# Optimization experiments

Measured on AMD Instinct MI355X. Metric: run time of the kernel, lower is better.

## Reference

```python
import jax, jax.numpy as jnp
import numpy as np

B, N, DEG, E, Hd, IT = 512, 81, 20, 16, 96, 4


def sudoku_neighbors():
    # 20 constraint neighbors (row/col/box, excluding self) per cell of a 9x9 grid
    n = 9
    nbrs = []
    for r in range(n):
        for c in range(n):
            s = set()
            for k in range(n):
                s.add(r * n + k)
                s.add(k * n + c)
            br, bc = (r // 3) * 3, (c // 3) * 3
            for dr in range(3):
                for dc in range(3):
                    s.add((br + dr) * n + (bc + dc))
            s.discard(r * n + c)
            nbrs.append(sorted(s))
    return np.asarray(nbrs, dtype=np.int32)  # [81, 20]


def mlp3(x, w1, b1, w2, b2, w3, b3):
    # MLP([in, h, h, out]): ReLU between layers, linear output
    x = jax.nn.relu(x @ w1 + b1)
    x = jax.nn.relu(x @ w2 + b2)
    return x @ w3 + b3


def setup_inputs() -> dict:
    key = jax.random.key(0)
    ks = iter(jax.random.split(key, 64))
    W = lambda shape, s=0.05: jax.random.normal(next(ks), shape, jnp.float32) * s
    inp = {
        'grids': jax.random.randint(next(ks), (B, N), 0, 10),
        'nbr': jnp.asarray(sudoku_neighbors()),
        'iters': IT,
        'c0': jax.random.normal(next(ks), (B * N, Hd), jnp.float32),
        'embed_w': W((10, E), 1.0),
        'in_w1': W((E, Hd)), 'in_b1': jnp.zeros((Hd,)),
        'in_w2': W((Hd, Hd)), 'in_b2': jnp.zeros((Hd,)),
        'in_w3': W((Hd, Hd)), 'in_b3': jnp.zeros((Hd,)),
        'f_w1': W((2 * Hd, Hd)), 'f_b1': jnp.zeros((Hd,)),
        'f_w2': W((Hd, Hd)), 'f_b2': jnp.zeros((Hd,)),
        'f_w3': W((Hd, Hd)), 'f_b3': jnp.zeros((Hd,)),
        'g_w1': W((2 * Hd, Hd)), 'g_b1': jnp.zeros((Hd,)),
        'g_w2': W((Hd, Hd)), 'g_b2': jnp.zeros((Hd,)),
        'g_w3': W((Hd, Hd)), 'g_b3': jnp.zeros((Hd,)),
        'lstm_wih': W((Hd, 4 * Hd)), 'lstm_whh': W((Hd, 4 * Hd)),
        'lstm_bih': jnp.zeros((4 * Hd,)), 'lstm_bhh': jnp.zeros((4 * Hd,)),
        'r_w1': W((Hd, Hd)), 'r_b1': jnp.zeros((Hd,)),
        'r_w2': W((Hd, Hd)), 'r_b2': jnp.zeros((Hd,)),
        'r_w3': W((Hd, E)), 'r_b3': jnp.zeros((E,)),
    }
    return inp


def reference(grids, nbr, iters, c0, embed_w,
              in_w1, in_b1, in_w2, in_b2, in_w3, in_b3,
              f_w1, f_b1, f_w2, f_b2, f_w3, f_b3,
              g_w1, g_b1, g_w2, g_b2, g_w3, g_b3,
              lstm_wih, lstm_whh, lstm_bih, lstm_bhh,
              r_w1, r_b1, r_w2, r_b2, r_w3, r_b3):
    X = mlp3(embed_w[grids], in_w1, in_b1, in_w2, in_b2, in_w3, in_b3)  # [B,N,Hd]
    h0 = jax.lax.stop_gradient(X).reshape(B * N, Hd)  # H = X.clone().detach()
    c = c0  # [B*N, Hd]

    def step(carry, _):
        h, c = carry
        H = h.reshape(B, N, Hd)
        Hn = H[:, nbr]  # gather neighbor states [B,N,DEG,Hd]
        pair = jnp.concatenate(
            [jnp.broadcast_to(H[:, :, None, :], Hn.shape), Hn], axis=-1)  # [B,N,DEG,2Hd]
        M = mlp3(pair, f_w1, f_b1, f_w2, f_b2, f_w3, f_b3).sum(axis=2)  # [B,N,Hd]
        x_in = mlp3(jnp.concatenate([X, M], axis=-1),
                    g_w1, g_b1, g_w2, g_b2, g_w3, g_b3).reshape(B * N, Hd)
        gates = x_in @ lstm_wih + lstm_bih + h @ lstm_whh + lstm_bhh
        i, f, g, o = jnp.split(gates, 4, axis=-1)  # torch gate order i,f,g,o
        c2 = jax.nn.sigmoid(f) * c + jax.nn.sigmoid(i) * jnp.tanh(g)
        h2 = jax.nn.sigmoid(o) * jnp.tanh(c2)
        out = mlp3(h2.reshape(B, N, Hd), r_w1, r_b1, r_w2, r_b2, r_w3, r_b3)
        return (h2, c2), out

    _, outs = jax.lax.scan(step, (h0, c), None, length=iters)
    return outs  # [iters, B, N, E]
```

## Files before the change

### kernel.cpp

```cpp
#include <hip/hip_runtime.h>
#include <math.h>

#define Bsz 512
#define Nc  81
#define Rtot (Bsz*Nc)
#define DEG 20
#define Edim 16
#define HD  96
#define NITER 4

typedef __attribute__((ext_vector_type(8))) __bf16 bf16x8;
typedef __attribute__((ext_vector_type(4))) float f32x4;

__device__ __forceinline__ float sigf(float x){ return 1.0f/(1.0f+__expf(-x)); }
__device__ __forceinline__ float tanh_fast(float x){ return 2.0f/(1.0f+__expf(-2.0f*x)) - 1.0f; }

__device__ __forceinline__ unsigned short f2bf(float f){
    union{float f; unsigned u;} v; v.f=f;
    unsigned r = v.u + 0x7fff + ((v.u>>16)&1);
    return (unsigned short)(r>>16);
}
__device__ __forceinline__ float bf2f(unsigned short s){
    union{unsigned u; float f;} v; v.u=((unsigned)s)<<16; return v.f;
}
__device__ __forceinline__ bf16x8 pack8f(const float* x){
    bf16x8 r;
    #pragma unroll
    for (int j=0;j<8;j++) r[j]=(__bf16)x[j];
    return r;
}
__device__ __forceinline__ bf16x8 ldw(const __bf16* p){ return *(const bf16x8*)p; }

__device__ __forceinline__ int swz(int row, int col){
    return row*96 + ((((col>>2) ^ (row&7))<<2) | (col&3));
}
__device__ __forceinline__ void ldtr8(const float* tp, int row, int c, float* o){
    const int r96 = row*96, rho = row&7;
    const float4 a = *(const float4*)(tp + r96 + ((((c>>2)  ) ^ rho)<<2));
    const float4 b = *(const float4*)(tp + r96 + ((((c>>2)+1) ^ rho)<<2));
    o[0]=a.x;o[1]=a.y;o[2]=a.z;o[3]=a.w;o[4]=b.x;o[5]=b.y;o[6]=b.z;o[7]=b.w;
}
__device__ __forceinline__ bf16x8 packtr8(const float* tp, int row, int c){
    float t[8]; ldtr8(tp,row,c,t); return pack8f(t);
}

#define OFF_FW1T 0
#define OFF_FW2T 18432
#define OFF_FW3T 27648
#define OFF_GW1T 36864
#define OFF_GW2T 55296
#define OFF_GW3T 64512
#define OFF_WIHT 73728
#define OFF_WHHT 110592
#define OFF_RW1T 147456
#define OFF_RW2T 156672
#define OFF_RW3T 165888
#define OFF_IW1T 167424
#define OFF_IW2T 170496
#define OFF_IW3T 179712
#define WT_TOTAL 188928

__global__ __launch_bounds__(256) void k_prep(
    const float* __restrict__ fw1, const float* __restrict__ fw2, const float* __restrict__ fw3,
    const float* __restrict__ gw1, const float* __restrict__ gw2, const float* __restrict__ gw3,
    const float* __restrict__ wih, const float* __restrict__ whh,
    const float* __restrict__ rw1, const float* __restrict__ rw2, const float* __restrict__ rw3,
    const float* __restrict__ iw1, const float* __restrict__ iw2, const float* __restrict__ iw3,
    __bf16* __restrict__ wt)
{
    int i = blockIdx.x*256 + threadIdx.x;
    if (i >= WT_TOTAL) return;
    int j = i;
    if (j < 18432){ int n=j/96, k=j-n*96;
        wt[OFF_FW1T+j] = (__bf16)(n<96 ? fw1[k*96+n] : fw1[(96+k)*96+(n-96)]); return; }
    j -= 18432;
    if (j < 9216){ int n=j/96, k=j-n*96; wt[OFF_FW2T+j]=(__bf16)fw2[k*96+n]; return; }
    j -= 9216;
    if (j < 9216){ int n=j/96, k=j-n*96; wt[OFF_FW3T+j]=(__bf16)fw3[k*96+n]; return; }
    j -= 9216;
    if (j < 18432){ int n=j/192, k=j-n*192; wt[OFF_GW1T+j]=(__bf16)gw1[k*96+n]; return; }
    j -= 18432;
    if (j < 9216){ int n=j/96, k=j-n*96; wt[OFF_GW2T+j]=(__bf16)gw2[k*96+n]; return; }
    j -= 9216;
    if (j < 9216){ int n=j/96, k=j-n*96; wt[OFF_GW3T+j]=(__bf16)gw3[k*96+n]; return; }
    j -= 9216;
    if (j < 36864){ int n=j/96, k=j-n*96; wt[OFF_WIHT+j]=(__bf16)wih[k*384+n]; return; }
    j -= 36864;
    if (j < 36864){ int n=j/96, k=j-n*96; wt[OFF_WHHT+j]=(__bf16)whh[k*384+n]; return; }
    j -= 36864;
    if (j < 9216){ int n=j/96, k=j-n*96; wt[OFF_RW1T+j]=(__bf16)rw1[k*96+n]; return; }
    j -= 9216;
    if (j < 9216){ int n=j/96, k=j-n*96; wt[OFF_RW2T+j]=(__bf16)rw2[k*96+n]; return; }
    j -= 9216;
    if (j < 1536){ int n=j/96, k=j-n*96; wt[OFF_RW3T+j]=(__bf16)rw3[k*16+n]; return; }
    j -= 1536;
    if (j < 3072){ int n=j>>5, k=j&31; wt[OFF_IW1T+j]=(__bf16)iw1[(k&15)*96+n]; return; }
    j -= 3072;
    if (j < 9216){ int n=j/96, k=j-n*96; wt[OFF_IW2T+j]=(__bf16)iw2[k*96+n]; return; }
    j -= 9216;
    { int n=j/96, k=j-n*96; wt[OFF_IW3T+j]=(__bf16)iw3[k*96+n]; }
}

__global__ __launch_bounds__(64) void k_embed2(
    const int* __restrict__ grids, const float* __restrict__ embw,
    const __bf16* __restrict__ wt,
    const float* __restrict__ ib1, const float* __restrict__ ib2, const float* __restrict__ ib3,
    __bf16* __restrict__ X, __bf16* __restrict__ Ag, __bf16* __restrict__ Bmg)
{
    __shared__ float tp[16*96];
    const int lane = threadIdx.x & 63;
    const int row16 = lane&15, kgrp = lane>>4, ko = kgrp*8;
    const int rowA = blockIdx.x*16 + row16;
    const int rowO = blockIdx.x*16 + kgrp*4;

    const __bf16* iw1t = wt + OFF_IW1T;
    const __bf16* iw2t = wt + OFF_IW2T;
    const __bf16* iw3t = wt + OFF_IW3T;
    const __bf16* fw1t = wt + OFF_FW1T;

    const int g = grids[rowA];
    const float* ew = embw + g*Edim + (kgrp&1)*8;
    bf16x8 ef;
    #pragma unroll
    for (int j=0;j<8;j++){
        float e = ew[j];
        if (kgrp < 2) ef[j] = (__bf16)e;
        else          ef[j] = (__bf16)(e - bf2f(f2bf(e)));
    }
    #pragma unroll
    for (int nf=0;nf<6;nf++){
        f32x4 c={0.f,0.f,0.f,0.f};
        c=__builtin_amdgcn_mfma_f32_16x16x32_bf16(ef, ldw(iw1t+(size_t)(nf*16+row16)*32+ko), c,0,0,0);
        float b=ib1[nf*16+row16];
        #pragma unroll
        for (int q=0;q<4;q++) tp[swz(kgrp*4+q, nf*16+row16)]=fmaxf(c[q]+b,0.f);
    }
    __syncthreads();
    bf16x8 ta[3];
    #pragma unroll
    for (int kf=0;kf<3;kf++) ta[kf]=packtr8(tp,row16,kf*32+ko);
    __syncthreads();
    #pragma unroll
    for (int nf=0;nf<6;nf++){
        f32x4 c={0.f,0.f,0.f,0.f};
        #pragma unroll
        for (int kf=0;kf<3;kf++)
            c=__builtin_amdgcn_mfma_f32_16x16x32_bf16(ta[kf], ldw(iw2t+(size_t)(nf*16+row16)*HD+kf*32+ko), c,0,0,0);
        float b=ib2[nf*16+row16];
        #pragma unroll
        for (int q=0;q<4;q++) tp[swz(kgrp*4+q, nf*16+row16)]=fmaxf(c[q]+b,0.f);
    }
    __syncthreads();
    #pragma unroll
    for (int kf=0;kf<3;kf++) ta[kf]=packtr8(tp,row16,kf*32+ko);
    __syncthreads();
    #pragma unroll
    for (int nf=0;nf<6;nf++){
        f32x4 c={0.f,0.f,0.f,0.f};
        #pragma unroll
        for (int kf=0;kf<3;kf++)
            c=__builtin_amdgcn_mfma_f32_16x16x32_bf16(ta[kf], ldw(iw3t+(size_t)(nf*16+row16)*HD+kf*32+ko), c,0,0,0);
        float b=ib3[nf*16+row16];
        #pragma unroll
        for (int q=0;q<4;q++){
            float v=c[q]+b;
            X[(size_t)(rowO+q)*HD + nf*16+row16]=(__bf16)v;
            tp[swz(kgrp*4+q, nf*16+row16)]=v;
        }
    }
    __syncthreads();
    bf16x8 hf[3];
    #pragma unroll
    for (int kf=0;kf<3;kf++) hf[kf]=packtr8(tp,row16,kf*32+ko);
    #pragma unroll
    for (int nf=0;nf<12;nf++){
        f32x4 c={0.f,0.f,0.f,0.f};
        #pragma unroll
        for (int kf=0;kf<3;kf++)
            c=__builtin_amdgcn_mfma_f32_16x16x32_bf16(hf[kf], ldw(fw1t+(size_t)(nf*16+row16)*HD+kf*32+ko), c,0,0,0);
        __bf16* dst = (nf<6)? Ag : Bmg;
        int col = ((nf<6)? nf : nf-6)*16 + row16;
        #pragma unroll
        for (int q=0;q<4;q++) dst[(size_t)(rowO+q)*HD+col]=(__bf16)c[q];
    }
}

__global__ __launch_bounds__(64) void k_edge(
    const __bf16* __restrict__ Ag, const __bf16* __restrict__ Bmg,
    const int* __restrict__ nbr,
    const float* __restrict__ fb1, const __bf16* __restrict__ fw2t,
    const float* __restrict__ fb2, const __bf16* __restrict__ fw3t,
    const float* __restrict__ fb3,
    __bf16* __restrict__ M)
{
    __shared__ float accs[16*96];
    const int lane = threadIdx.x & 63;
    const int row16 = lane&15, kgrp = lane>>4, ko = kgrp*8;
    const int rowA = blockIdx.x*16 + row16;
    const int iI = rowA % Nc;
    const __bf16* BmB = Bmg + (size_t)(rowA - iI)*HD + ko;

    bf16x8 w2f[3][6];
    #pragma unroll
    for (int kf=0; kf<3; kf++)
        #pragma unroll
        for (int nf=0; nf<6; nf++)
            w2f[kf][nf] = ldw(fw2t + (size_t)(nf*16+row16)*HD + kf*32+ko);

    float a[3][8];
    #pragma unroll
    for (int kf=0;kf<3;kf++){
        bf16x8 av = ldw(Ag + (size_t)rowA*HD + kf*32 + ko);
        #pragma unroll
        for (int j=0;j<8;j++) a[kf][j] = (float)av[j] + fb1[kf*32+ko+j];
    }
    float b2c[6], b3c[6];
    #pragma unroll
    for (int nf=0;nf<6;nf++){ b2c[nf]=fb2[nf*16+row16]; b3c[nf]=20.0f*fb3[nf*16+row16]; }

    f32x4 acc[6];
    #pragma unroll
    for (int nf=0;nf<6;nf++) acc[nf]=(f32x4){0.f,0.f,0.f,0.f};

    const int* nrow = nbr + iI*DEG;
    bf16x8 v0,v1,v2;
    {
        const __bf16* Vb = BmB + (size_t)nrow[0]*HD;
        v0=ldw(Vb); v1=ldw(Vb+32); v2=ldw(Vb+64);
    }
    #pragma unroll 2
    for (int d=0; d<DEG; d++){
        bf16x8 n0,n1,n2;
        {
            int dn = (d+1<DEG)? d+1 : 0;
            const __bf16* Vb = BmB + (size_t)nrow[dn]*HD;
            n0=ldw(Vb); n1=ldw(Vb+32); n2=ldw(Vb+64);
        }
        bf16x8 xf[3];
        {
            float t[8];
            #pragma unroll
            for (int jj=0;jj<8;jj++) t[jj]=fmaxf(a[0][jj]+(float)v0[jj],0.f);
            xf[0]=pack8f(t);
            #pragma unroll
            for (int jj=0;jj<8;jj++) t[jj]=fmaxf(a[1][jj]+(float)v1[jj],0.f);
            xf[1]=pack8f(t);
            #pragma unroll
            for (int jj=0;jj<8;jj++) t[jj]=fmaxf(a[2][jj]+(float)v2[jj],0.f);
            xf[2]=pack8f(t);
        }
        f32x4 c[6];
        #pragma unroll
        for (int nf=0;nf<6;nf++) c[nf]=(f32x4){0.f,0.f,0.f,0.f};
        #pragma unroll
        for (int kf=0;kf<3;kf++)
            #pragma unroll
            for (int nf=0;nf<6;nf++)
                c[nf]=__builtin_amdgcn_mfma_f32_16x16x32_bf16(xf[kf],w2f[kf][nf],c[nf],0,0,0);
        #pragma unroll
        for (int nf=0;nf<6;nf++)
            #pragma unroll
            for (int q2=0;q2<4;q2++)
                acc[nf][q2]+=fmaxf(c[nf][q2]+b2c[nf],0.f);
        v0=n0; v1=n1; v2=n2;
    }

    #pragma unroll
    for (int nf=0;nf<6;nf++)
        #pragma unroll
        for (int q2=0;q2<4;q2++)
            accs[swz(kgrp*4+q2, nf*16+row16)]=acc[nf][q2];
    __syncthreads();

    f32x4 c2[6];
    #pragma unroll
    for (int nf=0;nf<6;nf++) c2[nf]=(f32x4){0.f,0.f,0.f,0.f};
    #pragma unroll
    for (int kf=0;kf<3;kf++){
        float h[8]; ldtr8(accs, row16, kf*32+ko, h);
        bf16x8 hif, lof;
        #pragma unroll
        for (int j=0;j<8;j++){
            unsigned short hs=f2bf(h[j]);
            union{unsigned short s; __bf16 b;} u; u.s=hs;
            hif[j]=u.b; lof[j]=(__bf16)(h[j]-bf2f(hs));
        }
        #pragma unroll
        for (int nf=0;nf<6;nf++){
            bf16x8 w3f = ldw(fw3t + (size_t)(nf*16+row16)*HD + kf*32+ko);
            c2[nf]=__builtin_amdgcn_mfma_f32_16x16x32_bf16(hif,w3f,c2[nf],0,0,0);
            c2[nf]=__builtin_amdgcn_mfma_f32_16x16x32_bf16(lof,w3f,c2[nf],0,0,0);
        }
    }
    const int rowOut = blockIdx.x*16 + kgrp*4;
    #pragma unroll
    for (int nf=0;nf<6;nf++)
        #pragma unroll
        for (int q2=0;q2<4;q2++)
            M[(size_t)(rowOut+q2)*HD + nf*16+row16] = (__bf16)(c2[nf][q2]+b3c[nf]);
}

__global__ __launch_bounds__(64) void k_fused(
    const __bf16* __restrict__ Xg, const __bf16* __restrict__ Mg,
    const __bf16* __restrict__ Hin, __bf16* __restrict__ Hout,
    const float* __restrict__ Cin, float* __restrict__ Cout,
    __bf16* __restrict__ Ag, __bf16* __restrict__ Bmg,
    const __bf16* __restrict__ wt,
    const float* __restrict__ gb1, const float* __restrict__ gb2, const float* __restrict__ gb3,
    const float* __restrict__ bih, const float* __restrict__ bhh,
    const float* __restrict__ rb1, const float* __restrict__ rb2, const float* __restrict__ rb3,
    float* __restrict__ out, int it, int wab)
{
    __shared__ float tp[16*96];
    const int lane = threadIdx.x & 63;
    const int row16 = lane&15, kgrp = lane>>4, ko = kgrp*8;
    const int rowA = blockIdx.x*16 + row16;
    const int rowO = blockIdx.x*16 + kgrp*4;

    const __bf16* fw1t = wt + OFF_FW1T;
    const __bf16* gw1t = wt + OFF_GW1T;
    const __bf16* gw2t = wt + OFF_GW2T;
    const __bf16* gw3t = wt + OFF_GW3T;
    const __bf16* wiht = wt + OFF_WIHT;
    const __bf16* whht = wt + OFF_WHHT;
    const __bf16* rw1t = wt + OFF_RW1T;
    const __bf16* rw2t = wt + OFF_RW2T;
    const __bf16* rw3t = wt + OFF_RW3T;

    bf16x8 xm[6];
    #pragma unroll
    for (int kf=0;kf<3;kf++){
        xm[kf]   = ldw(Xg + (size_t)rowA*HD + kf*32+ko);
        xm[3+kf] = ldw(Mg + (size_t)rowA*HD + kf*32+ko);
    }
    #pragma unroll
    for (int nf=0;nf<6;nf++){
        f32x4 c={0.f,0.f,0.f,0.f};
        #pragma unroll
        for (int kf=0;kf<6;kf++)
            c=__builtin_amdgcn_mfma_f32_16x16x32_bf16(xm[kf], ldw(gw1t+(size_t)(nf*16+row16)*192+kf*32+ko), c,0,0,0);
        float b=gb1[nf*16+row16];
        #pragma unroll
        for (int q=0;q<4;q++) tp[swz(kgrp*4+q, nf*16+row16)]=fmaxf(c[q]+b,0.f);
    }
    __syncthreads();
    bf16x8 ta[3];
    #pragma unroll
    for (int kf=0;kf<3;kf++) ta[kf]=packtr8(tp,row16,kf*32+ko);
    __syncthreads();
    #pragma unroll
    for (int nf=0;nf<6;nf++){
        f32x4 c={0.f,0.f,0.f,0.f};
        #pragma unroll
        for (int kf=0;kf<3;kf++)
            c=__builtin_amdgcn_mfma_f32_16x16x32_bf16(ta[kf], ldw(gw2t+(size_t)(nf*16+row16)*HD+kf*32+ko), c,0,0,0);
        float b=gb2[nf*16+row16];
        #pragma unroll
        for (int q=0;q<4;q++) tp[swz(kgrp*4+q, nf*16+row16)]=fmaxf(c[q]+b,0.f);
    }
    __syncthreads();
    #pragma unroll
    for (int kf=0;kf<3;kf++) ta[kf]=packtr8(tp,row16,kf*32+ko);
    __syncthreads();
    #pragma unroll
    for (int nf=0;nf<6;nf++){
        f32x4 c={0.f,0.f,0.f,0.f};
        #pragma unroll
        for (int kf=0;kf<3;kf++)
            c=__builtin_amdgcn_mfma_f32_16x16x32_bf16(ta[kf], ldw(gw3t+(size_t)(nf*16+row16)*HD+kf*32+ko), c,0,0,0);
        float b=gb3[nf*16+row16];
        #pragma unroll
        for (int q=0;q<4;q++) tp[swz(kgrp*4+q, nf*16+row16)]=c[q]+b;
    }
    __syncthreads();
    bf16x8 xf[3];
    #pragma unroll
    for (int kf=0;kf<3;kf++) xf[kf]=packtr8(tp,row16,kf*32+ko);
    __syncthreads();

    bf16x8 hfa[3];
    #pragma unroll
    for (int kf=0;kf<3;kf++) hfa[kf]=ldw(Hin + (size_t)rowA*HD + kf*32+ko);

    #pragma unroll 2
    for (int nf=0;nf<6;nf++){
        const int col = nf*16+row16;
        f32x4 g4[4];
        #pragma unroll
        for (int g=0;g<4;g++) g4[g]=(f32x4){0.f,0.f,0.f,0.f};
        #pragma unroll
        for (int g=0;g<4;g++){
            #pragma unroll
            for (int kf=0;kf<3;kf++){
                const int kk = kf*32+ko;
                g4[g]=__builtin_amdgcn_mfma_f32_16x16x32_bf16(xf[kf],  ldw(wiht+(size_t)(g*96+col)*HD+kk), g4[g],0,0,0);
                g4[g]=__builtin_amdgcn_mfma_f32_16x16x32_bf16(hfa[kf], ldw(whht+(size_t)(g*96+col)*HD+kk), g4[g],0,0,0);
            }
        }
        float bi=bih[    col]+bhh[    col];
        float bf=bih[ 96+col]+bhh[ 96+col];
        float bg=bih[192+col]+bhh[192+col];
        float bo=bih[288+col]+bhh[288+col];
        #pragma unroll
        for (int q=0;q<4;q++){
            size_t idx=(size_t)(rowO+q)*HD+col;
            float cold=Cin[idx];
            float iv=sigf(g4[0][q]+bi), fv=sigf(g4[1][q]+bf);
            float gv=tanh_fast(g4[2][q]+bg), ov=sigf(g4[3][q]+bo);
            float c2v=fv*cold+iv*gv;
            float h2v=ov*tanh_fast(c2v);
            Cout[idx]=c2v; Hout[idx]=(__bf16)h2v;
            tp[swz(kgrp*4+q,col)]=h2v;
        }
    }
    __syncthreads();

    bf16x8 hf[3];
    #pragma unroll
    for (int kf=0;kf<3;kf++) hf[kf]=packtr8(tp,row16,kf*32+ko);
    __syncthreads();

    if (wab){
        #pragma unroll
        for (int nf=0;nf<12;nf++){
            f32x4 c={0.f,0.f,0.f,0.f};
            #pragma unroll
            for (int kf=0;kf<3;kf++)
                c=__builtin_amdgcn_mfma_f32_16x16x32_bf16(hf[kf], ldw(fw1t+(size_t)(nf*16+row16)*HD+kf*32+ko), c,0,0,0);
            __bf16* dst = (nf<6)? Ag : Bmg;
            int col = ((nf<6)? nf : nf-6)*16 + row16;
            #pragma unroll
            for (int q=0;q<4;q++) dst[(size_t)(rowO+q)*HD+col]=(__bf16)c[q];
        }
    }

    #pragma unroll
    for (int nf=0;nf<6;nf++){
        f32x4 c={0.f,0.f,0.f,0.f};
        #pragma unroll
        for (int kf=0;kf<3;kf++)
            c=__builtin_amdgcn_mfma_f32_16x16x32_bf16(hf[kf], ldw(rw1t+(size_t)(nf*16+row16)*HD+kf*32+ko), c,0,0,0);
        float b=rb1[nf*16+row16];
        #pragma unroll
        for (int q=0;q<4;q++) tp[swz(kgrp*4+q, nf*16+row16)]=fmaxf(c[q]+b,0.f);
    }
    __syncthreads();
    #pragma unroll
    for (int kf=0;kf<3;kf++) ta[kf]=packtr8(tp,row16,kf*32+ko);
    __syncthreads();
    #pragma unroll
    for (int nf=0;nf<6;nf++){
        f32x4 c={0.f,0.f,0.f,0.f};
        #pragma unroll
        for (int kf=0;kf<3;kf++)
            c=__builtin_amdgcn_mfma_f32_16x16x32_bf16(ta[kf], ldw(rw2t+(size_t)(nf*16+row16)*HD+kf*32+ko), c,0,0,0);
        float b=rb2[nf*16+row16];
        #pragma unroll
        for (int q=0;q<4;q++) tp[swz(kgrp*4+q, nf*16+row16)]=fmaxf(c[q]+b,0.f);
    }
    __syncthreads();
    #pragma unroll
    for (int kf=0;kf<3;kf++) ta[kf]=packtr8(tp,row16,kf*32+ko);
    {
        f32x4 c={0.f,0.f,0.f,0.f};
        #pragma unroll
        for (int kf=0;kf<3;kf++)
            c=__builtin_amdgcn_mfma_f32_16x16x32_bf16(ta[kf], ldw(rw3t+(size_t)row16*HD+kf*32+ko), c,0,0,0);
        float b=rb3[row16];
        #pragma unroll
        for (int q=0;q<4;q++)
            out[((size_t)it*Rtot + rowO+q)*Edim + row16]=c[q]+b;
    }
}

extern "C" void kernel_launch(void* const* d_in, const int* in_sizes, int n_in,
                              void* d_out, int out_size, void* d_ws, size_t ws_size,
                              hipStream_t stream) {
    const int*   grids  = (const int*)  d_in[0];
    const int*   nbr    = (const int*)  d_in[1];
    const float* c0     = (const float*)d_in[3];
    const float* embw   = (const float*)d_in[4];
    const float* in_w1  = (const float*)d_in[5];
    const float* in_b1  = (const float*)d_in[6];
    const float* in_w2  = (const float*)d_in[7];
    const float* in_b2  = (const float*)d_in[8];
    const float* in_w3  = (const float*)d_in[9];
    const float* in_b3  = (const float*)d_in[10];
    const float* f_w1   = (const float*)d_in[11];
    const float* f_b1   = (const float*)d_in[12];
    const float* f_w2   = (const float*)d_in[13];
    const float* f_b2   = (const float*)d_in[14];
    const float* f_w3   = (const float*)d_in[15];
    const float* f_b3   = (const float*)d_in[16];
    const float* g_w1   = (const float*)d_in[17];
    const float* g_b1   = (const float*)d_in[18];
    const float* g_w2   = (const float*)d_in[19];
    const float* g_b2   = (const float*)d_in[20];
    const float* g_w3   = (const float*)d_in[21];
    const float* g_b3   = (const float*)d_in[22];
    const float* wih    = (const float*)d_in[23];
    const float* whh    = (const float*)d_in[24];
    const float* bih    = (const float*)d_in[25];
    const float* bhh    = (const float*)d_in[26];
    const float* r_w1   = (const float*)d_in[27];
    const float* r_b1   = (const float*)d_in[28];
    const float* r_w2   = (const float*)d_in[29];
    const float* r_b2   = (const float*)d_in[30];
    const float* r_w3   = (const float*)d_in[31];
    const float* r_b3   = (const float*)d_in[32];

    __bf16* Xb = (__bf16*)d_ws;
    __bf16* Hb = Xb + (size_t)Rtot*HD;
    float*  Cw = (float*)(Hb + (size_t)Rtot*HD);
    __bf16* Aa = (__bf16*)(Cw + (size_t)Rtot*HD);
    __bf16* Bm = Aa + (size_t)Rtot*HD;
    __bf16* Mm = Bm + (size_t)Rtot*HD;
    __bf16* wt = Mm + (size_t)Rtot*HD;
    float* out = (float*)d_out;

    const __bf16* fw2t = wt + OFF_FW2T;
    const __bf16* fw3t = wt + OFF_FW3T;

    hipLaunchKernelGGL(k_prep, dim3((WT_TOTAL+255)/256), dim3(256), 0, stream,
        f_w1, f_w2, f_w3, g_w1, g_w2, g_w3, wih, whh, r_w1, r_w2, r_w3,
        in_w1, in_w2, in_w3, wt);

    hipLaunchKernelGGL(k_embed2, dim3(Rtot/16), dim3(64), 0, stream,
        grids, embw, wt, in_b1, in_b2, in_b3, Xb, Aa, Bm);

    for (int it=0; it<NITER; ++it){
        hipLaunchKernelGGL(k_edge, dim3(Rtot/16), dim3(64), 0, stream,
            Aa, Bm, nbr, f_b1, fw2t, f_b2, fw3t, f_b3, Mm);
        hipLaunchKernelGGL(k_fused, dim3(Rtot/16), dim3(64), 0, stream,
            Xb, Mm,
            (it==0)? Xb : Hb, Hb,
            (it==0)? c0 : Cw, Cw,
            Aa, Bm, wt,
            g_b1, g_b2, g_b3, bih, bhh, r_b1, r_b2, r_b3,
            out, it, (it<NITER-1)?1:0);
    }
}
```

Before: 506.0 us.

## Stage padded weights in LDS and share across four waves in fused kernel

The per-node fused kernel now runs 256-thread blocks covering 64 rows, with four waves sharing weight tiles that are copied cooperatively into LDS. A new prep kernel writes the weights with rows padded to 104 elements to avoid bank conflicts. The LSTM gates are computed one at a time so only two gate matrices sit in LDS at once. This replaces repeated per-wave global or L2 weight fetches with shared LDS reads, at the cost of extra block-wide barriers, staging copies and higher LDS use that may limit occupancy.

```diff
diff --git a/kernel.cpp b/kernel.cpp
--- a/kernel.cpp
+++ b/kernel.cpp
@@ -59,6 +59,18 @@
 #define OFF_IW2T 170496
 #define OFF_IW3T 179712
 #define WT_TOTAL 188928
+
+#define P_GW1A 0
+#define P_GW1B 9984
+#define P_GW2  19968
+#define P_GW3  29952
+#define P_WIH0 39936
+#define P_WHH0 79872
+#define P_FW1  119808
+#define P_RW1  139776
+#define P_RW2  149760
+#define P_RW3  159744
+#define P_TOTAL 161408
 
 __global__ __launch_bounds__(256) void k_prep(
     const float* __restrict__ fw1, const float* __restrict__ fw2, const float* __restrict__ fw3,
@@ -101,6 +113,39 @@
     { int n=j/96, k=j-n*96; wt[OFF_IW3T+j]=(__bf16)iw3[k*96+n]; }
 }
 
+__global__ __launch_bounds__(256) void k_prep2(
+    const float* __restrict__ gw1, const float* __restrict__ gw2, const float* __restrict__ gw3,
+    const float* __restrict__ wih, const float* __restrict__ whh, const float* __restrict__ fw1,
+    const float* __restrict__ rw1, const float* __restrict__ rw2, const float* __restrict__ rw3,
+    __bf16* __restrict__ wp)
+{
+    int i = blockIdx.x*256 + threadIdx.x;
+    if (i >= P_TOTAL) return;
+    int j = i;
+    if (j < 9984){ int o=j/104, k=j-o*104; wp[i]=(__bf16)((k<96)? gw1[k*96+o] : 0.f); return; }
+    j -= 9984;
+    if (j < 9984){ int o=j/104, k=j-o*104; wp[i]=(__bf16)((k<96)? gw1[(96+k)*96+o] : 0.f); return; }
+    j -= 9984;
+    if (j < 9984){ int o=j/104, k=j-o*104; wp[i]=(__bf16)((k<96)? gw2[k*96+o] : 0.f); return; }
+    j -= 9984;
+    if (j < 9984){ int o=j/104, k=j-o*104; wp[i]=(__bf16)((k<96)? gw3[k*96+o] : 0.f); return; }
+    j -= 9984;
+    if (j < 39936){ int g=j/9984, r=j-g*9984; int o=r/104, k=r-o*104;
+        wp[i]=(__bf16)((k<96)? wih[k*384 + g*96 + o] : 0.f); return; }
+    j -= 39936;
+    if (j < 39936){ int g=j/9984, r=j-g*9984; int o=r/104, k=r-o*104;
+        wp[i]=(__bf16)((k<96)? whh[k*384 + g*96 + o] : 0.f); return; }
+    j -= 39936;
+    if (j < 19968){ int o=j/104, k=j-o*104;
+        wp[i]=(__bf16)((k>=96)? 0.f : (o<96 ? fw1[k*96+o] : fw1[(96+k)*96+(o-96)])); return; }
+    j -= 19968;
+    if (j < 9984){ int o=j/104, k=j-o*104; wp[i]=(__bf16)((k<96)? rw1[k*96+o]:0.f); return; }
+    j -= 9984;
+    if (j < 9984){ int o=j/104, k=j-o*104; wp[i]=(__bf16)((k<96)? rw2[k*96+o]:0.f); return; }
+    j -= 9984;
+    { int o=j/104, k=j-o*104; wp[i]=(__bf16)((k<96)? rw3[k*16+o]:0.f); }
+}
+
 __global__ __launch_bounds__(64) void k_embed2(
     const int* __restrict__ grids, const float* __restrict__ embw,
     const __bf16* __restrict__ wt,
@@ -300,172 +345,232 @@
             M[(size_t)(rowOut+q2)*HD + nf*16+row16] = (__bf16)(c2[nf][q2]+b3c[nf]);
 }
 
-__global__ __launch_bounds__(64) void k_fused(
+__device__ __forceinline__ void stageW(const __bf16* __restrict__ src, __bf16* dst, int nelem){
+    const int4* s=(const int4*)src; int4* d=(int4*)dst;
+    const int n = nelem>>3;
+    for (int i=threadIdx.x; i<n; i+=256) d[i]=s[i];
+}
+__device__ __forceinline__ bf16x8 ldl(const __bf16* w, int row, int kk){
+    return *(const bf16x8*)(w + row*104 + kk);
+}
+
+__global__ __launch_bounds__(256,2) void k_fused256(
     const __bf16* __restrict__ Xg, const __bf16* __restrict__ Mg,
     const __bf16* __restrict__ Hin, __bf16* __restrict__ Hout,
     const float* __restrict__ Cin, float* __restrict__ Cout,
     __bf16* __restrict__ Ag, __bf16* __restrict__ Bmg,
-    const __bf16* __restrict__ wt,
+    const __bf16* __restrict__ wp,
     const float* __restrict__ gb1, const float* __restrict__ gb2, const float* __restrict__ gb3,
     const float* __restrict__ bih, const float* __restrict__ bhh,
     const float* __restrict__ rb1, const float* __restrict__ rb2, const float* __restrict__ rb3,
     float* __restrict__ out, int it, int wab)
 {
-    __shared__ float tp[16*96];
-    const int lane = threadIdx.x & 63;
-    const int row16 = lane&15, kgrp = lane>>4, ko = kgrp*8;
-    const int rowA = blockIdx.x*16 + row16;
-    const int rowO = blockIdx.x*16 + kgrp*4;
-
-    const __bf16* fw1t = wt + OFF_FW1T;
-    const __bf16* gw1t = wt + OFF_GW1T;
-    const __bf16* gw2t = wt + OFF_GW2T;
-    const __bf16* gw3t = wt + OFF_GW3T;
-    const __bf16* wiht = wt + OFF_WIHT;
-    const __bf16* whht = wt + OFF_WHHT;
-    const __bf16* rw1t = wt + OFF_RW1T;
-    const __bf16* rw2t = wt + OFF_RW2T;
-    const __bf16* rw3t = wt + OFF_RW3T;
-
-    bf16x8 xm[6];
+    __shared__ __align__(16) __bf16 wl[19968];
+    __shared__ float tp4[4][16*96];
+    const int tid = threadIdx.x;
+    const int wave = tid>>6, lane = tid&63;
+    const int row16=lane&15, kgrp=lane>>4, ko=kgrp*8;
+    const int rowA = blockIdx.x*64 + wave*16 + row16;
+    const int rowO = blockIdx.x*64 + wave*16 + kgrp*4;
+    float* tp = tp4[wave];
+
+    bf16x8 xm[3], mm[3], hfa[3];
     #pragma unroll
     for (int kf=0;kf<3;kf++){
-        xm[kf]   = ldw(Xg + (size_t)rowA*HD + kf*32+ko);
-        xm[3+kf] = ldw(Mg + (size_t)rowA*HD + kf*32+ko);
-    }
-    #pragma unroll
-    for (int nf=0;nf<6;nf++){
-        f32x4 c={0.f,0.f,0.f,0.f};
-        #pragma unroll
-        for (int kf=0;kf<6;kf++)
-            c=__builtin_amdgcn_mfma_f32_16x16x32_bf16(xm[kf], ldw(gw1t+(size_t)(nf*16+row16)*192+kf*32+ko), c,0,0,0);
-        float b=gb1[nf*16+row16];
-        #pragma unroll
-        for (int q=0;q<4;q++) tp[swz(kgrp*4+q, nf*16+row16)]=fmaxf(c[q]+b,0.f);
+        xm[kf]  = ldw(Xg  + (size_t)rowA*HD + kf*32+ko);
+        mm[kf]  = ldw(Mg  + (size_t)rowA*HD + kf*32+ko);
+        hfa[kf] = ldw(Hin + (size_t)rowA*HD + kf*32+ko);
+    }
+
+    f32x4 acc[6];
+
+    stageW(wp+P_GW1A, wl, 9984); __syncthreads();
+    #pragma unroll
+    for (int nf=0;nf<6;nf++){
+        f32x4 c={0.f,0.f,0.f,0.f};
+        const int row=nf*16+row16;
+        #pragma unroll
+        for (int kf=0;kf<3;kf++) c=__builtin_amdgcn_mfma_f32_16x16x32_bf16(xm[kf], ldl(wl,row,kf*32+ko), c,0,0,0);
+        acc[nf]=c;
+    }
+    __syncthreads(); stageW(wp+P_GW1B, wl, 9984); __syncthreads();
+    #pragma unroll
+    for (int nf=0;nf<6;nf++){
+        f32x4 c=acc[nf];
+        const int row=nf*16+row16;
+        #pragma unroll
+        for (int kf=0;kf<3;kf++) c=__builtin_amdgcn_mfma_f32_16x16x32_bf16(mm[kf], ldl(wl,row,kf*32+ko), c,0,0,0);
+        float b=gb1[row];
+        #pragma unroll
+        for (int q=0;q<4;q++) tp[swz(kgrp*4+q,row)]=fmaxf(c[q]+b,0.f);
     }
     __syncthreads();
     bf16x8 ta[3];
     #pragma unroll
     for (int kf=0;kf<3;kf++) ta[kf]=packtr8(tp,row16,kf*32+ko);
-    __syncthreads();
-    #pragma unroll
-    for (int nf=0;nf<6;nf++){
-        f32x4 c={0.f,0.f,0.f,0.f};
-        #pragma unroll
-        for (int kf=0;kf<3;kf++)
-            c=__builtin_amdgcn_mfma_f32_16x16x32_bf16(ta[kf], ldw(gw2t+(size_t)(nf*16+row16)*HD+kf*32+ko), c,0,0,0);
-        float b=gb2[nf*16+row16];
-        #pragma unroll
-        for (int q=0;q<4;q++) tp[swz(kgrp*4+q, nf*16+row16)]=fmaxf(c[q]+b,0.f);
+    stageW(wp+P_GW2, wl, 9984);
+    __syncthreads();
+    #pragma unroll
+    for (int nf=0;nf<6;nf++){
+        f32x4 c={0.f,0.f,0.f,0.f};
+        const int row=nf*16+row16;
+        #pragma unroll
+        for (int kf=0;kf<3;kf++) c=__builtin_amdgcn_mfma_f32_16x16x32_bf16(ta[kf], ldl(wl,row,kf*32+ko), c,0,0,0);
+        float b=gb2[row];
+        #pragma unroll
+        for (int q=0;q<4;q++) tp[swz(kgrp*4+q,row)]=fmaxf(c[q]+b,0.f);
     }
     __syncthreads();
     #pragma unroll
     for (int kf=0;kf<3;kf++) ta[kf]=packtr8(tp,row16,kf*32+ko);
-    __syncthreads();
-    #pragma unroll
-    for (int nf=0;nf<6;nf++){
-        f32x4 c={0.f,0.f,0.f,0.f};
-        #pragma unroll
-        for (int kf=0;kf<3;kf++)
-            c=__builtin_amdgcn_mfma_f32_16x16x32_bf16(ta[kf], ldw(gw3t+(size_t)(nf*16+row16)*HD+kf*32+ko), c,0,0,0);
-        float b=gb3[nf*16+row16];
-        #pragma unroll
-        for (int q=0;q<4;q++) tp[swz(kgrp*4+q, nf*16+row16)]=c[q]+b;
+    stageW(wp+P_GW3, wl, 9984);
+    __syncthreads();
+    #pragma unroll
+    for (int nf=0;nf<6;nf++){
+        f32x4 c={0.f,0.f,0.f,0.f};
+        const int row=nf*16+row16;
+        #pragma unroll
+        for (int kf=0;kf<3;kf++) c=__builtin_amdgcn_mfma_f32_16x16x32_bf16(ta[kf], ldl(wl,row,kf*32+ko), c,0,0,0);
+        float b=gb3[row];
+        #pragma unroll
+        for (int q=0;q<4;q++) tp[swz(kgrp*4+q,row)]=c[q]+b;
     }
     __syncthreads();
     bf16x8 xf[3];
     #pragma unroll
     for (int kf=0;kf<3;kf++) xf[kf]=packtr8(tp,row16,kf*32+ko);
-    __syncthreads();
-
-    bf16x8 hfa[3];
-    #pragma unroll
-    for (int kf=0;kf<3;kf++) hfa[kf]=ldw(Hin + (size_t)rowA*HD + kf*32+ko);
-
-    #pragma unroll 2
-    for (int nf=0;nf<6;nf++){
-        const int col = nf*16+row16;
-        f32x4 g4[4];
-        #pragma unroll
-        for (int g=0;g<4;g++) g4[g]=(f32x4){0.f,0.f,0.f,0.f};
-        #pragma unroll
-        for (int g=0;g<4;g++){
-            #pragma unroll
-            for (int kf=0;kf<3;kf++){
-                const int kk = kf*32+ko;
-                g4[g]=__builtin_amdgcn_mfma_f32_16x16x32_bf16(xf[kf],  ldw(wiht+(size_t)(g*96+col)*HD+kk), g4[g],0,0,0);
-                g4[g]=__builtin_amdgcn_mfma_f32_16x16x32_bf16(hfa[kf], ldw(whht+(size_t)(g*96+col)*HD+kk), g4[g],0,0,0);
-            }
-        }
-        float bi=bih[    col]+bhh[    col];
-        float bf=bih[ 96+col]+bhh[ 96+col];
-        float bg=bih[192+col]+bhh[192+col];
-        float bo=bih[288+col]+bhh[288+col];
+    stageW(wp+P_WIH0+0*9984, wl, 9984); stageW(wp+P_WHH0+0*9984, wl+9984, 9984);
+    __syncthreads();
+    float st[6][4];
+    float cold[6][4];
+    #pragma unroll
+    for (int nf=0;nf<6;nf++)
+        #pragma unroll
+        for (int q=0;q<4;q++) cold[nf][q]=Cin[(size_t)(rowO+q)*HD + nf*16+row16];
+    #pragma unroll
+    for (int nf=0;nf<6;nf++){
+        f32x4 c={0.f,0.f,0.f,0.f};
+        const int row=nf*16+row16;
+        #pragma unroll
+        for (int kf=0;kf<3;kf++){
+            c=__builtin_amdgcn_mfma_f32_16x16x32_bf16(xf[kf],  ldl(wl,      row,kf*32+ko), c,0,0,0);
+            c=__builtin_amdgcn_mfma_f32_16x16x32_bf16(hfa[kf], ldl(wl+9984, row,kf*32+ko), c,0,0,0);
+        }
+        float b=bih[row]+bhh[row];
+        #pragma unroll
+        for (int q=0;q<4;q++) st[nf][q]=sigf(c[q]+b);
+    }
+    __syncthreads();
+    stageW(wp+P_WIH0+2*9984, wl, 9984); stageW(wp+P_WHH0+2*9984, wl+9984, 9984);
+    __syncthreads();
+    #pragma unroll
+    for (int nf=0;nf<6;nf++){
+        f32x4 c={0.f,0.f,0.f,0.f};
+        const int row=nf*16+row16;
+        #pragma unroll
+        for (int kf=0;kf<3;kf++){
+            c=__builtin_amdgcn_mfma_f32_16x16x32_bf16(xf[kf],  ldl(wl,      row,kf*32+ko), c,0,0,0);
+            c=__builtin_amdgcn_mfma_f32_16x16x32_bf16(hfa[kf], ldl(wl+9984, row,kf*32+ko), c,0,0,0);
+        }
+        float b=bih[192+row]+bhh[192+row];
+        #pragma unroll
+        for (int q=0;q<4;q++) st[nf][q]=st[nf][q]*tanh_fast(c[q]+b);
+    }
+    __syncthreads();
+    stageW(wp+P_WIH0+1*9984, wl, 9984); stageW(wp+P_WHH0+1*9984, wl+9984, 9984);
+    __syncthreads();
+    float cacc[6][4];
+    #pragma unroll
+    for (int nf=0;nf<6;nf++){
+        f32x4 c={0.f,0.f,0.f,0.f};
+        const int row=nf*16+row16;
+        #pragma unroll
+        for (int kf=0;kf<3;kf++){
+            c=__builtin_amdgcn_mfma_f32_16x16x32_bf16(xf[kf],  ldl(wl,      row,kf*32+ko), c,0,0,0);
+            c=__builtin_amdgcn_mfma_f32_16x16x32_bf16(hfa[kf], ldl(wl+9984, row,kf*32+ko), c,0,0,0);
+        }
+        float b=bih[96+row]+bhh[96+row];
+        #pragma unroll
+        for (int q=0;q<4;q++) cacc[nf][q]=sigf(c[q]+b)*cold[nf][q]+st[nf][q];
+    }
+    __syncthreads();
+    stageW(wp+P_WIH0+3*9984, wl, 9984); stageW(wp+P_WHH0+3*9984, wl+9984, 9984);
+    __syncthreads();
+    #pragma unroll
+    for (int nf=0;nf<6;nf++){
+        f32x4 c={0.f,0.f,0.f,0.f};
+        const int row=nf*16+row16;
+        #pragma unroll
+        for (int kf=0;kf<3;kf++){
+            c=__builtin_amdgcn_mfma_f32_16x16x32_bf16(xf[kf],  ldl(wl,      row,kf*32+ko), c,0,0,0);
+            c=__builtin_amdgcn_mfma_f32_16x16x32_bf16(hfa[kf], ldl(wl+9984, row,kf*32+ko), c,0,0,0);
+        }
+        float b=bih[288+row]+bhh[288+row];
         #pragma unroll
         for (int q=0;q<4;q++){
-            size_t idx=(size_t)(rowO+q)*HD+col;
-            float cold=Cin[idx];
-            float iv=sigf(g4[0][q]+bi), fv=sigf(g4[1][q]+bf);
-            float gv=tanh_fast(g4[2][q]+bg), ov=sigf(g4[3][q]+bo);
-            float c2v=fv*cold+iv*gv;
-            float h2v=ov*tanh_fast(c2v);
+            size_t idx=(size_t)(rowO+q)*HD+row;
+            float c2v=cacc[nf][q];
+            float h2v=sigf(c[q]+b)*tanh_fast(c2v);
             Cout[idx]=c2v; Hout[idx]=(__bf16)h2v;
-            tp[swz(kgrp*4+q,col)]=h2v;
-        }
-    }
-    __syncthreads();
-
+            tp[swz(kgrp*4+q,row)]=h2v;
+        }
+    }
+    __syncthreads();
     bf16x8 hf[3];
     #pragma unroll
     for (int kf=0;kf<3;kf++) hf[kf]=packtr8(tp,row16,kf*32+ko);
-    __syncthreads();
-
+    if (wab) stageW(wp+P_FW1, wl, 19968);
+    __syncthreads();
     if (wab){
         #pragma unroll
         for (int nf=0;nf<12;nf++){
             f32x4 c={0.f,0.f,0.f,0.f};
+            const int row=nf*16+row16;
             #pragma unroll
-            for (int kf=0;kf<3;kf++)
-                c=__builtin_amdgcn_mfma_f32_16x16x32_bf16(hf[kf], ldw(fw1t+(size_t)(nf*16+row16)*HD+kf*32+ko), c,0,0,0);
+            for (int kf=0;kf<3;kf++) c=__builtin_amdgcn_mfma_f32_16x16x32_bf16(hf[kf], ldl(wl,row,kf*32+ko), c,0,0,0);
             __bf16* dst = (nf<6)? Ag : Bmg;
             int col = ((nf<6)? nf : nf-6)*16 + row16;
             #pragma unroll
             for (int q=0;q<4;q++) dst[(size_t)(rowO+q)*HD+col]=(__bf16)c[q];
         }
     }
-
-    #pragma unroll
-    for (int nf=0;nf<6;nf++){
-        f32x4 c={0.f,0.f,0.f,0.f};
-        #pragma unroll
-        for (int kf=0;kf<3;kf++)
-            c=__builtin_amdgcn_mfma_f32_16x16x32_bf16(hf[kf], ldw(rw1t+(size_t)(nf*16+row16)*HD+kf*32+ko), c,0,0,0);
-        float b=rb1[nf*16+row16];
-        #pragma unroll
-        for (int q=0;q<4;q++) tp[swz(kgrp*4+q, nf*16+row16)]=fmaxf(c[q]+b,0.f);
+    __syncthreads();
+    stageW(wp+P_RW1, wl, 9984);
+    __syncthreads();
+    #pragma unroll
+    for (int nf=0;nf<6;nf++){
+        f32x4 c={0.f,0.f,0.f,0.f};
+        const int row=nf*16+row16;
+        #pragma unroll
+        for (int kf=0;kf<3;kf++) c=__builtin_amdgcn_mfma_f32_16x16x32_bf16(hf[kf], ldl(wl,row,kf*32+ko), c,0,0,0);
+        float b=rb1[row];
+        #pragma unroll
+        for (int q=0;q<4;q++) tp[swz(kgrp*4+q,row)]=fmaxf(c[q]+b,0.f);
     }
     __syncthreads();
     #pragma unroll
     for (int kf=0;kf<3;kf++) ta[kf]=packtr8(tp,row16,kf*32+ko);
-    __syncthreads();
-    #pragma unroll
-    for (int nf=0;nf<6;nf++){
-        f32x4 c={0.f,0.f,0.f,0.f};
-        #pragma unroll
-        for (int kf=0;kf<3;kf++)
-            c=__builtin_amdgcn_mfma_f32_16x16x32_bf16(ta[kf], ldw(rw2t+(size_t)(nf*16+row16)*HD+kf*32+ko), c,0,0,0);
-        float b=rb2[nf*16+row16];
-        #pragma unroll
-        for (int q=0;q<4;q++) tp[swz(kgrp*4+q, nf*16+row16)]=fmaxf(c[q]+b,0.f);
+    stageW(wp+P_RW2, wl, 9984);
+    __syncthreads();
+    #pragma unroll
+    for (int nf=0;nf<6;nf++){
+        f32x4 c={0.f,0.f,0.f,0.f};
+        const int row=nf*16+row16;
+        #pragma unroll
+        for (int kf=0;kf<3;kf++) c=__builtin_amdgcn_mfma_f32_16x16x32_bf16(ta[kf], ldl(wl,row,kf*32+ko), c,0,0,0);
+        float b=rb2[row];
+        #pragma unroll
+        for (int q=0;q<4;q++) tp[swz(kgrp*4+q,row)]=fmaxf(c[q]+b,0.f);
     }
     __syncthreads();
     #pragma unroll
     for (int kf=0;kf<3;kf++) ta[kf]=packtr8(tp,row16,kf*32+ko);
+    stageW(wp+P_RW3, wl, 1664);
+    __syncthreads();
     {
         f32x4 c={0.f,0.f,0.f,0.f};
         #pragma unroll
-        for (int kf=0;kf<3;kf++)
-            c=__builtin_amdgcn_mfma_f32_16x16x32_bf16(ta[kf], ldw(rw3t+(size_t)row16*HD+kf*32+ko), c,0,0,0);
+        for (int kf=0;kf<3;kf++) c=__builtin_amdgcn_mfma_f32_16x16x32_bf16(ta[kf], ldl(wl,row16,kf*32+ko), c,0,0,0);
         float b=rb3[row16];
         #pragma unroll
         for (int q=0;q<4;q++)
@@ -516,6 +621,7 @@
     __bf16* Bm = Aa + (size_t)Rtot*HD;
     __bf16* Mm = Bm + (size_t)Rtot*HD;
     __bf16* wt = Mm + (size_t)Rtot*HD;
+    __bf16* wpad = wt + WT_TOTAL;
     float* out = (float*)d_out;
 
     const __bf16* fw2t = wt + OFF_FW2T;
@@ -524,6 +630,8 @@
     hipLaunchKernelGGL(k_prep, dim3((WT_TOTAL+255)/256), dim3(256), 0, stream,
         f_w1, f_w2, f_w3, g_w1, g_w2, g_w3, wih, whh, r_w1, r_w2, r_w3,
         in_w1, in_w2, in_w3, wt);
+    hipLaunchKernelGGL(k_prep2, dim3((P_TOTAL+255)/256), dim3(256), 0, stream,
+        g_w1, g_w2, g_w3, wih, whh, f_w1, r_w1, r_w2, r_w3, wpad);
 
     hipLaunchKernelGGL(k_embed2, dim3(Rtot/16), dim3(64), 0, stream,
         grids, embw, wt, in_b1, in_b2, in_b3, Xb, Aa, Bm);
@@ -531,11 +639,11 @@
     for (int it=0; it<NITER; ++it){
         hipLaunchKernelGGL(k_edge, dim3(Rtot/16), dim3(64), 0, stream,
             Aa, Bm, nbr, f_b1, fw2t, f_b2, fw3t, f_b3, Mm);
-        hipLaunchKernelGGL(k_fused, dim3(Rtot/16), dim3(64), 0, stream,
+        hipLaunchKernelGGL(k_fused256, dim3(Rtot/64), dim3(256), 0, stream,
             Xb, Mm,
             (it==0)? Xb : Hb, Hb,
             (it==0)? c0 : Cw, Cw,
-            Aa, Bm, wt,
+            Aa, Bm, wpad,
             g_b1, g_b2, g_b3, bih, bhh, r_b1, r_b2, r_b3,
             out, it, (it<NITER-1)?1:0);
     }
```

After: 501.8 us. About the same (-0.8%).
